# Kernel tuning notes

Measured on AMD Instinct MI355X. Metric: run time of the kernel, lower is better.

## Reference

```python
import jax, jax.numpy as jnp
import numpy as np

ALPHA = 0.2  # leaky_relu negative slope
NEG_INF = -1e18


def setup_inputs() -> dict:
    key = jax.random.key(0)
    ks = jax.random.split(key, 7)
    B, N, E = 32, 1024, 768
    OUT, MLP = 256, 2
    sent_emb = jax.random.normal(ks[0], (B, N, E), dtype=jnp.float32)
    batch_e = jnp.sort(jax.random.randint(ks[1], (B, 4), 0, N), axis=-1)
    # xavier-ish scaled weights
    W_w = jax.random.normal(ks[2], (OUT, E), dtype=jnp.float32) * (1.0 / np.sqrt(E))
    W_b = jax.random.normal(ks[3], (OUT,), dtype=jnp.float32) * 0.02
    a_w = jax.random.normal(ks[4], (1, 2 * OUT), dtype=jnp.float32) * (1.0 / np.sqrt(2 * OUT))
    mlp_w = jax.random.normal(ks[5], (MLP, OUT), dtype=jnp.float32) * (1.0 / np.sqrt(OUT))
    mlp_b = jax.random.normal(ks[6], (MLP,), dtype=jnp.float32) * 0.02
    return {"sent_emb": sent_emb, "batch_e": batch_e, "W_w": W_w, "W_b": W_b,
            "a_w": a_w, "mlp_w": mlp_w, "mlp_b": mlp_b}


def reference(sent_emb, batch_e, W_w, W_b, a_w, mlp_w, mlp_b):
    B, N, E = sent_emb.shape
    OUT = W_w.shape[0]
    # Wh = W(sent_emb): [B, N, OUT]
    Wh = jnp.einsum('bne,oe->bno', sent_emb, W_w) + W_b
    # a_T([H1 || H2]) decomposes: a1 . Wh_i + a2 . Wh_j (avoids [N,N,2*OUT] concat)
    a1, a2 = a_w[0, :OUT], a_w[0, OUT:]
    s1 = Wh @ a1  # [B, N]
    s2 = Wh @ a2  # [B, N]
    e = jax.nn.leaky_relu(s1[:, :, None] + s2[:, None, :], negative_slope=ALPHA)  # [B,N,N]
    # event mask: 0.9 inside [e1s,e1e)x[e2s,e2e), 0.1 elsewhere (both > 0, kept for fidelity)
    idx = jnp.arange(N)
    row_in = (idx[None, :] >= batch_e[:, 0:1]) & (idx[None, :] < batch_e[:, 1:2])  # [B,N]
    col_in = (idx[None, :] >= batch_e[:, 2:3]) & (idx[None, :] < batch_e[:, 3:4])  # [B,N]
    event_mask = jnp.where(row_in[:, :, None] & col_in[:, None, :], 0.9, 0.1)
    masked_e = jnp.where(event_mask > 0, e, NEG_INF)
    attn = jax.nn.softmax(masked_e, axis=-1)  # [B,N,N]
    h_prime = jax.nn.elu(jnp.einsum('bnm,bmo->bno', attn, Wh))  # [B,N,OUT]
    pooled = jnp.mean(h_prime, axis=1)  # avg_pooling over nodes -> [B,OUT]
    return pooled @ mlp_w.T + mlp_b  # [B, mlp_size]
```

## Files before the change

### kernel.cpp

```cpp
#include <hip/hip_runtime.h>
#include <hip/hip_bf16.h>

#define LOG2E 1.4426950408889634f

typedef short bfrag8 __attribute__((ext_vector_type(8)));
typedef float accf4 __attribute__((ext_vector_type(4)));

__device__ __forceinline__ unsigned pack2(float a, float b) {
    __hip_bfloat162 h = __float22bfloat162_rn(make_float2(a, b));
    return *(unsigned*)&h;
}
__device__ __forceinline__ float bflo(unsigned u) { return __uint_as_float(u << 16); }
__device__ __forceinline__ float bfhi(unsigned u) { return __uint_as_float(u & 0xFFFF0000u); }

__device__ __forceinline__ void gload_lds16(const void* g, void* lds) {
    __builtin_amdgcn_global_load_lds(
        (const __attribute__((address_space(1))) unsigned int*)g,
        (__attribute__((address_space(3))) unsigned int*)lds, 16, 0, 0);
}

__global__ __launch_bounds__(256) void convW_kernel(
    const float* __restrict__ Ww, unsigned short* __restrict__ WwB)
{
    const int id = (blockIdx.x * 256 + threadIdx.x) * 8;
    float4 a = *(const float4*)&Ww[id];
    float4 b = *(const float4*)&Ww[id + 4];
    uint4 pk;
    pk.x = pack2(a.x, a.y); pk.y = pack2(a.z, a.w);
    pk.z = pack2(b.x, b.y); pk.w = pack2(b.z, b.w);
    *(uint4*)&WwB[id] = pk;
}

__global__ __launch_bounds__(512) void gemm1_kernel(
    const float* __restrict__ sent, const unsigned short* __restrict__ WwB,
    const float* __restrict__ Wb, const float* __restrict__ aw,
    unsigned short* __restrict__ WhT, float* __restrict__ s1g,
    float* __restrict__ s2g)
{
    __shared__ char SMEM[131072];
    const int brow = blockIdx.x;
    const int t = threadIdx.x;
    const int lane = t & 63, w = t >> 6;
    const int wr = w >> 2, wc = w & 3;
    const int l15 = lane & 15, l4 = lane >> 4;
    const float* abase = sent + (size_t)brow * 128 * 768;

    accf4 acc[4][4];
#pragma unroll
    for (int i = 0; i < 4; ++i)
#pragma unroll
        for (int j = 0; j < 4; ++j)
            acc[i][j] = (accf4){0.f, 0.f, 0.f, 0.f};

    auto STAGE = [&](int buf, int k0) {
#pragma unroll
        for (int q = 0; q < 4; ++q) {
            const int id = (q << 9) + t;
            const int row = id >> 4, c = id & 15;
            gload_lds16(abase + (size_t)row * 768 + k0 + ((c ^ (row & 15)) << 2),
                        SMEM + (buf << 15) + (id << 4));
        }
#pragma unroll
        for (int q = 0; q < 4; ++q) {
            const int id = (q << 9) + t;
            const int col = id >> 3, c = id & 7;
            gload_lds16(WwB + (size_t)col * 768 + k0 + ((c ^ (col & 7)) << 3),
                        SMEM + 65536 + (buf << 15) + (id << 4));
        }
    };

    auto COMPUTE = [&](int buf) {
        const float* Ab = (const float*)(SMEM + (buf << 15));
        const unsigned short* Bb = (const unsigned short*)(SMEM + 65536 + (buf << 15));
#pragma unroll
        for (int kk = 0; kk < 2; ++kk) {
            bfrag8 af[4], bf[4];
#pragma unroll
            for (int mi = 0; mi < 4; ++mi) {
                const int row = (wr << 6) + (mi << 4) + l15;
                const int s0 = (kk << 3) + (l4 << 1);
                float4 a0 = *(const float4*)(Ab + (row << 6) + ((s0 ^ (row & 15)) << 2));
                float4 a1 = *(const float4*)(Ab + (row << 6) + (((s0 + 1) ^ (row & 15)) << 2));
                uint4 pk;
                pk.x = pack2(a0.x, a0.y); pk.y = pack2(a0.z, a0.w);
                pk.z = pack2(a1.x, a1.y); pk.w = pack2(a1.z, a1.w);
                af[mi] = *(bfrag8*)&pk;
            }
#pragma unroll
            for (int ni = 0; ni < 4; ++ni) {
                const int col = (wc << 6) + (ni << 4) + l15;
                const int s = (kk << 2) + l4;
                bf[ni] = *(const bfrag8*)(Bb + (col << 6) + ((s ^ (col & 7)) << 3));
            }
#pragma unroll
            for (int mi = 0; mi < 4; ++mi)
#pragma unroll
                for (int ni = 0; ni < 4; ++ni)
                    acc[mi][ni] = __builtin_amdgcn_mfma_f32_16x16x32_bf16(
                        af[mi], bf[ni], acc[mi][ni], 0, 0, 0);
        }
    };

    STAGE(0, 0);
    __syncthreads();
    for (int it = 0; it < 12; ++it) {
        if (it < 11) STAGE((it + 1) & 1, (it + 1) << 6);
        COMPUTE(it & 1);
        __syncthreads();
    }

    unsigned short (*T)[136] = (unsigned short(*)[136])SMEM;
    float (*sb1)[4] = (float(*)[4])(SMEM + 98304);
    float (*sb2)[4] = (float(*)[4])(SMEM + 100352);
    float sp1[16], sp2[16];
#pragma unroll
    for (int i = 0; i < 16; ++i) { sp1[i] = 0.f; sp2[i] = 0.f; }
#pragma unroll
    for (int ni = 0; ni < 4; ++ni) {
        const int colL = (wc << 6) + (ni << 4) + l15;
        const float wb  = Wb[colL];
        const float a1c = aw[colL] * LOG2E;
        const float a2c = aw[256 + colL] * LOG2E;
#pragma unroll
        for (int mi = 0; mi < 4; ++mi) {
            const int rowL = (wr << 6) + (mi << 4) + (l4 << 2);
            float v0 = acc[mi][ni][0] + wb, v1 = acc[mi][ni][1] + wb;
            float v2 = acc[mi][ni][2] + wb, v3 = acc[mi][ni][3] + wb;
            uint2 pk; pk.x = pack2(v0, v1); pk.y = pack2(v2, v3);
            *(uint2*)&T[colL][rowL] = pk;
            sp1[mi * 4 + 0] += v0 * a1c; sp1[mi * 4 + 1] += v1 * a1c;
            sp1[mi * 4 + 2] += v2 * a1c; sp1[mi * 4 + 3] += v3 * a1c;
            sp2[mi * 4 + 0] += v0 * a2c; sp2[mi * 4 + 1] += v1 * a2c;
            sp2[mi * 4 + 2] += v2 * a2c; sp2[mi * 4 + 3] += v3 * a2c;
        }
    }
#pragma unroll
    for (int d = 1; d < 16; d <<= 1)
#pragma unroll
        for (int i = 0; i < 16; ++i) {
            sp1[i] += __shfl_xor(sp1[i], d);
            sp2[i] += __shfl_xor(sp2[i], d);
        }
    if (l15 == 0)
#pragma unroll
        for (int mi = 0; mi < 4; ++mi)
#pragma unroll
            for (int reg = 0; reg < 4; ++reg) {
                const int rowL = (wr << 6) + (mi << 4) + (l4 << 2) + reg;
                sb1[rowL][wc] = sp1[mi * 4 + reg];
                sb2[rowL][wc] = sp2[mi * 4 + reg];
            }
    __syncthreads();
    {
        const int b = brow >> 3, m0 = (brow & 7) << 7;
        const int col = t >> 1, half = t & 1;
        unsigned short* dst = &WhT[(((size_t)b * 256 + col) << 10) + m0 + (half << 6)];
        const unsigned short* srcT = &T[col][half << 6];
#pragma unroll
        for (int q = 0; q < 8; ++q)
            *(uint4*)(dst + (q << 3)) = *(const uint4*)(srcT + (q << 3));
    }
    if (t < 128) {
        const int grow = brow * 128 + t;
        s1g[grow] = sb1[t][0] + sb1[t][1] + sb1[t][2] + sb1[t][3];
        s2g[grow] = sb2[t][0] + sb2[t][1] + sb2[t][2] + sb2[t][3];
    }
}

__global__ __launch_bounds__(512) void flash_kernel(
    const unsigned short* __restrict__ WhT, const float* __restrict__ s1g,
    const float* __restrict__ s2g, float* __restrict__ ppart)
{
    __shared__ char SMEM[98304];
    __shared__ float s2s[1024];
    __shared__ float zfull[128];
    __shared__ float wred[8];
    __shared__ float psum[2][256];
    const int bid0 = blockIdx.x;
    const int wg = ((bid0 & 7) << 5) + (bid0 >> 3);
    const int b = wg >> 3, nt = wg & 7, n0 = nt << 7;
    const int t = threadIdx.x;
    const int lane = t & 63, w = t >> 6;
    const int wr = w >> 2, wc = w & 3;
    const int l15 = lane & 15, l4 = lane >> 4;
    const int prow = t >> 2, pc0 = (t & 3) << 1;
    const unsigned short* wbase = WhT + ((size_t)b << 18);

    {
        const int i = t << 1;
        *(float2*)&s2s[i] = *(const float2*)&s2g[(b << 10) + i];
    }
    auto STAGEB = [&](int buf, int m0) {
#pragma unroll
        for (int q = 0; q < 4; ++q) {
            const int id = (q << 9) + t;
            const int col = id >> 3, c = id & 7;
            gload_lds16(wbase + ((size_t)col << 10) + m0 + ((c ^ (col & 7)) << 3),
                        SMEM + (buf << 15) + (id << 4));
        }
    };
    STAGEB(0, 0);
    const float s1r = s1g[(b << 10) + n0 + prow];
    __syncthreads();
    float mm = fmaxf(s2s[t], s2s[t + 512]);
#pragma unroll
    for (int d = 1; d < 64; d <<= 1) mm = fmaxf(mm, __shfl_xor(mm, d));
    if (lane == 0) wred[w] = mm;
    __syncthreads();
    float s2mx = wred[0];
#pragma unroll
    for (int i = 1; i < 8; ++i) s2mx = fmaxf(s2mx, wred[i]);
    const float xm = s1r + s2mx;
    const float Mr = fmaxf(xm, 0.2f * xm);

    accf4 acc[4][4];
#pragma unroll
    for (int i = 0; i < 4; ++i)
#pragma unroll
        for (int j = 0; j < 4; ++j)
            acc[i][j] = (accf4){0.f, 0.f, 0.f, 0.f};
    float zp = 0.f;

    auto PCOMP = [&](int buf, int mt) {
        const float* sp = &s2s[(mt << 6) + (pc0 << 3)];
        float4 x0 = *(const float4*)sp;
        float4 x1 = *(const float4*)(sp + 4);
        float4 x2 = *(const float4*)(sp + 8);
        float4 x3 = *(const float4*)(sp + 12);
        float xs[16] = {x0.x, x0.y, x0.z, x0.w, x1.x, x1.y, x1.z, x1.w,
                        x2.x, x2.y, x2.z, x2.w, x3.x, x3.y, x3.z, x3.w};
        unsigned u[8];
#pragma unroll
        for (int j = 0; j < 8; ++j) {
            float a = s1r + xs[2 * j], c = s1r + xs[2 * j + 1];
            a = fmaxf(a, 0.2f * a) - Mr;
            c = fmaxf(c, 0.2f * c) - Mr;
            u[j] = pack2(__builtin_amdgcn_exp2f(a), __builtin_amdgcn_exp2f(c));
            zp += bflo(u[j]) + bfhi(u[j]);
        }
        char* pb = SMEM + 65536 + (buf << 14) + (prow << 7);
        uint4 k0; k0.x = u[0]; k0.y = u[1]; k0.z = u[2]; k0.w = u[3];
        uint4 k1; k1.x = u[4]; k1.y = u[5]; k1.z = u[6]; k1.w = u[7];
        *(uint4*)(pb + ((pc0 ^ (prow & 7)) << 4)) = k0;
        *(uint4*)(pb + (((pc0 + 1) ^ (prow & 7)) << 4)) = k1;
    };
    auto MM = [&](int buf) {
        const unsigned short* Bb = (const unsigned short*)(SMEM + (buf << 15));
        const char* Pb = SMEM + 65536 + (buf << 14);
#pragma unroll
        for (int kk = 0; kk < 2; ++kk) {
            bfrag8 af[4], bf[4];
#pragma unroll
            for (int mi = 0; mi < 4; ++mi) {
                const int row = (wr << 6) + (mi << 4) + l15;
                const int s = (kk << 2) + l4;
                af[mi] = *(const bfrag8*)(Pb + (row << 7) + ((s ^ (row & 7)) << 4));
            }
#pragma unroll
            for (int ni = 0; ni < 4; ++ni) {
                const int col = (wc << 6) + (ni << 4) + l15;
                const int s = (kk << 2) + l4;
                bf[ni] = *(const bfrag8*)(Bb + (col << 6) + ((s ^ (col & 7)) << 3));
            }
#pragma unroll
            for (int mi = 0; mi < 4; ++mi)
#pragma unroll
                for (int ni = 0; ni < 4; ++ni)
                    acc[mi][ni] = __builtin_amdgcn_mfma_f32_16x16x32_bf16(
                        af[mi], bf[ni], acc[mi][ni], 0, 0, 0);
        }
    };

    PCOMP(0, 0);
    __syncthreads();
    for (int mt = 0; mt < 16; ++mt) {
        if (mt < 15) {
            STAGEB((mt + 1) & 1, (mt + 1) << 6);
            PCOMP((mt + 1) & 1, mt + 1);
        }
        MM(mt & 1);
        __syncthreads();
    }

    zp += __shfl_xor(zp, 1);
    zp += __shfl_xor(zp, 2);
    if ((lane & 3) == 0) zfull[prow] = zp;
    __syncthreads();

    float rz[16];
#pragma unroll
    for (int mi = 0; mi < 4; ++mi)
#pragma unroll
        for (int r = 0; r < 4; ++r)
            rz[mi * 4 + r] = 1.0f / zfull[(wr << 6) + (mi << 4) + (l4 << 2) + r];
#pragma unroll
    for (int ni = 0; ni < 4; ++ni) {
        float cs = 0.f;
#pragma unroll
        for (int mi = 0; mi < 4; ++mi)
#pragma unroll
            for (int r = 0; r < 4; ++r) {
                float v = acc[mi][ni][r] * rz[mi * 4 + r];
                cs += v > 0.f ? v : (__expf(v) - 1.0f);
            }
        cs += __shfl_xor(cs, 16);
        cs += __shfl_xor(cs, 32);
        if (l4 == 0) psum[wr][(wc << 6) + (ni << 4) + l15] = cs;
    }
    __syncthreads();
    if (t < 256)
        ppart[(((size_t)b << 3) + nt) * 256 + t] = psum[0][t] + psum[1][t];
}

__global__ __launch_bounds__(256) void final_kernel(
    const float* __restrict__ ppart, const float* __restrict__ mlpw,
    const float* __restrict__ mlpb, float* __restrict__ out)
{
    __shared__ float r0[4], r1[4];
    const int b = blockIdx.x, t = threadIdx.x;
    float p = 0.f;
#pragma unroll
    for (int nt = 0; nt < 8; ++nt)
        p += ppart[(((size_t)b << 3) + nt) * 256 + t];
    float m0 = p * mlpw[t], m1 = p * mlpw[256 + t];
#pragma unroll
    for (int d = 1; d < 64; d <<= 1) {
        m0 += __shfl_xor(m0, d);
        m1 += __shfl_xor(m1, d);
    }
    if ((t & 63) == 0) { r0[t >> 6] = m0; r1[t >> 6] = m1; }
    __syncthreads();
    if (t == 0) out[b * 2 + 0] = (r0[0] + r0[1] + r0[2] + r0[3]) * (1.f / 1024.f) + mlpb[0];
    if (t == 1) out[b * 2 + 1] = (r1[0] + r1[1] + r1[2] + r1[3]) * (1.f / 1024.f) + mlpb[1];
}

extern "C" void kernel_launch(void* const* d_in, const int* in_sizes, int n_in,
                              void* d_out, int out_size, void* d_ws, size_t ws_size,
                              hipStream_t stream) {
    const float* sent = (const float*)d_in[0];
    const float* Ww   = (const float*)d_in[2];
    const float* Wb   = (const float*)d_in[3];
    const float* aw   = (const float*)d_in[4];
    const float* mlpw = (const float*)d_in[5];
    const float* mlpb = (const float*)d_in[6];
    float* out = (float*)d_out;

    char* ws = (char*)d_ws;
    unsigned short* WhT  = (unsigned short*)ws;
    unsigned short* WwB  = (unsigned short*)(ws + 16777216);
    float*          s1g  = (float*)(ws + 17170432);
    float*          s2g  = s1g + 32768;
    float*          ppart= s2g + 32768;

    convW_kernel<<<96, 256, 0, stream>>>(Ww, WwB);
    gemm1_kernel<<<256, 512, 0, stream>>>(sent, WwB, Wb, aw, WhT, s1g, s2g);
    flash_kernel<<<256, 512, 0, stream>>>(WhT, s1g, s2g, ppart);
    final_kernel<<<32, 256, 0, stream>>>(ppart, mlpw, mlpb, out);
}
```

Baseline: 204.2 us.

## Drop weight conversion kernel; convert to bf16 in registers before LDS staging

Removes the separate convW kernel and reads fp32 W directly in gemm1. A and W tiles are now loaded into registers, packed to bf16, and written to LDS, replacing the direct global-to-LDS async loads of fp32 A. This halves LDS footprint and removes per-MFMA fp32->bf16 conversion from LDS reads, at the cost of register-staged loads that are less asynchronous. Each block re-reads and re-converts fp32 W, so W traffic doubles per block.

Result: slower. 219.0 us (+7.3%).

```diff
diff --git a/kernel.cpp b/kernel.cpp
--- a/kernel.cpp
+++ b/kernel.cpp
@@ -19,25 +19,13 @@
         (__attribute__((address_space(3))) unsigned int*)lds, 16, 0, 0);
 }
 
-__global__ __launch_bounds__(256) void convW_kernel(
-    const float* __restrict__ Ww, unsigned short* __restrict__ WwB)
-{
-    const int id = (blockIdx.x * 256 + threadIdx.x) * 8;
-    float4 a = *(const float4*)&Ww[id];
-    float4 b = *(const float4*)&Ww[id + 4];
-    uint4 pk;
-    pk.x = pack2(a.x, a.y); pk.y = pack2(a.z, a.w);
-    pk.z = pack2(b.x, b.y); pk.w = pack2(b.z, b.w);
-    *(uint4*)&WwB[id] = pk;
-}
-
 __global__ __launch_bounds__(512) void gemm1_kernel(
-    const float* __restrict__ sent, const unsigned short* __restrict__ WwB,
+    const float* __restrict__ sent, const float* __restrict__ Ww,
     const float* __restrict__ Wb, const float* __restrict__ aw,
     unsigned short* __restrict__ WhT, float* __restrict__ s1g,
     float* __restrict__ s2g)
 {
-    __shared__ char SMEM[131072];
+    __shared__ char SMEM[98304];
     const int brow = blockIdx.x;
     const int t = threadIdx.x;
     const int lane = t & 63, w = t >> 6;
@@ -45,6 +33,9 @@
     const int l15 = lane & 15, l4 = lane >> 4;
     const float* abase = sent + (size_t)brow * 128 * 768;
 
+    const int ar = t >> 2, ac2 = (t & 3) << 1;
+    const int bc = t >> 1, bh = t & 1;
+
     accf4 acc[4][4];
 #pragma unroll
     for (int i = 0; i < 4; ++i)
@@ -52,45 +43,55 @@
         for (int j = 0; j < 4; ++j)
             acc[i][j] = (accf4){0.f, 0.f, 0.f, 0.f};
 
-    auto STAGE = [&](int buf, int k0) {
+    float4 aL[4], bL[8];
+    auto LOADR = [&](int k0) {
+        const float* ap = abase + ar * 768 + k0 + (ac2 << 3);
+#pragma unroll
+        for (int q = 0; q < 4; ++q) aL[q] = *(const float4*)(ap + (q << 2));
+        const float* bp = Ww + bc * 768 + k0 + (bh << 5);
+#pragma unroll
+        for (int q = 0; q < 8; ++q) bL[q] = *(const float4*)(bp + (q << 2));
+    };
+    auto WRITE = [&](int buf) {
+        char* Asb = SMEM + (buf << 14);
+#pragma unroll
+        for (int q = 0; q < 2; ++q) {
+            uint4 pk;
+            pk.x = pack2(aL[2 * q].x, aL[2 * q].y);
+            pk.y = pack2(aL[2 * q].z, aL[2 * q].w);
+            pk.z = pack2(aL[2 * q + 1].x, aL[2 * q + 1].y);
+            pk.w = pack2(aL[2 * q + 1].z, aL[2 * q + 1].w);
+            const int c = ac2 + q;
+            *(uint4*)(Asb + (ar << 7) + ((c ^ (ar & 7)) << 4)) = pk;
+        }
+        char* Bsb = SMEM + 32768 + (buf << 15);
 #pragma unroll
         for (int q = 0; q < 4; ++q) {
-            const int id = (q << 9) + t;
-            const int row = id >> 4, c = id & 15;
-            gload_lds16(abase + (size_t)row * 768 + k0 + ((c ^ (row & 15)) << 2),
-                        SMEM + (buf << 15) + (id << 4));
-        }
-#pragma unroll
-        for (int q = 0; q < 4; ++q) {
-            const int id = (q << 9) + t;
-            const int col = id >> 3, c = id & 7;
-            gload_lds16(WwB + (size_t)col * 768 + k0 + ((c ^ (col & 7)) << 3),
-                        SMEM + 65536 + (buf << 15) + (id << 4));
-        }
-    };
-
+            uint4 pk;
+            pk.x = pack2(bL[2 * q].x, bL[2 * q].y);
+            pk.y = pack2(bL[2 * q].z, bL[2 * q].w);
+            pk.z = pack2(bL[2 * q + 1].x, bL[2 * q + 1].y);
+            pk.w = pack2(bL[2 * q + 1].z, bL[2 * q + 1].w);
+            const int c = (bh << 2) + q;
+            *(uint4*)(Bsb + (bc << 7) + ((c ^ (bc & 7)) << 4)) = pk;
+        }
+    };
     auto COMPUTE = [&](int buf) {
-        const float* Ab = (const float*)(SMEM + (buf << 15));
-        const unsigned short* Bb = (const unsigned short*)(SMEM + 65536 + (buf << 15));
+        const char* Ab = SMEM + (buf << 14);
+        const char* Bb = SMEM + 32768 + (buf << 15);
 #pragma unroll
         for (int kk = 0; kk < 2; ++kk) {
+            const int s = (kk << 2) + l4;
             bfrag8 af[4], bf[4];
 #pragma unroll
             for (int mi = 0; mi < 4; ++mi) {
                 const int row = (wr << 6) + (mi << 4) + l15;
-                const int s0 = (kk << 3) + (l4 << 1);
-                float4 a0 = *(const float4*)(Ab + (row << 6) + ((s0 ^ (row & 15)) << 2));
-                float4 a1 = *(const float4*)(Ab + (row << 6) + (((s0 + 1) ^ (row & 15)) << 2));
-                uint4 pk;
-                pk.x = pack2(a0.x, a0.y); pk.y = pack2(a0.z, a0.w);
-                pk.z = pack2(a1.x, a1.y); pk.w = pack2(a1.z, a1.w);
-                af[mi] = *(bfrag8*)&pk;
+                af[mi] = *(const bfrag8*)(Ab + (row << 7) + ((s ^ (row & 7)) << 4));
             }
 #pragma unroll
             for (int ni = 0; ni < 4; ++ni) {
                 const int col = (wc << 6) + (ni << 4) + l15;
-                const int s = (kk << 2) + l4;
-                bf[ni] = *(const bfrag8*)(Bb + (col << 6) + ((s ^ (col & 7)) << 3));
+                bf[ni] = *(const bfrag8*)(Bb + (col << 7) + ((s ^ (col & 7)) << 4));
             }
 #pragma unroll
             for (int mi = 0; mi < 4; ++mi)
@@ -101,17 +102,19 @@
         }
     };
 
-    STAGE(0, 0);
+    LOADR(0);
+    WRITE(0);
     __syncthreads();
     for (int it = 0; it < 12; ++it) {
-        if (it < 11) STAGE((it + 1) & 1, (it + 1) << 6);
+        if (it < 11) LOADR((it + 1) << 6);
         COMPUTE(it & 1);
+        if (it < 11) WRITE((it + 1) & 1);
         __syncthreads();
     }
 
     unsigned short (*T)[136] = (unsigned short(*)[136])SMEM;
-    float (*sb1)[4] = (float(*)[4])(SMEM + 98304);
-    float (*sb2)[4] = (float(*)[4])(SMEM + 100352);
+    float (*sb1)[4] = (float(*)[4])(SMEM + 90112);
+    float (*sb2)[4] = (float(*)[4])(SMEM + 92160);
     float sp1[16], sp2[16];
 #pragma unroll
     for (int i = 0; i < 16; ++i) { sp1[i] = 0.f; sp2[i] = 0.f; }
@@ -245,22 +248,21 @@
         *(uint4*)(pb + (((pc0 + 1) ^ (prow & 7)) << 4)) = k1;
     };
     auto MM = [&](int buf) {
-        const unsigned short* Bb = (const unsigned short*)(SMEM + (buf << 15));
+        const char* Bb = SMEM + (buf << 15);
         const char* Pb = SMEM + 65536 + (buf << 14);
 #pragma unroll
         for (int kk = 0; kk < 2; ++kk) {
+            const int s = (kk << 2) + l4;
             bfrag8 af[4], bf[4];
 #pragma unroll
             for (int mi = 0; mi < 4; ++mi) {
                 const int row = (wr << 6) + (mi << 4) + l15;
-                const int s = (kk << 2) + l4;
                 af[mi] = *(const bfrag8*)(Pb + (row << 7) + ((s ^ (row & 7)) << 4));
             }
 #pragma unroll
             for (int ni = 0; ni < 4; ++ni) {
                 const int col = (wc << 6) + (ni << 4) + l15;
-                const int s = (kk << 2) + l4;
-                bf[ni] = *(const bfrag8*)(Bb + (col << 6) + ((s ^ (col & 7)) << 3));
+                bf[ni] = *(const bfrag8*)(Bb + (col << 7) + ((s ^ (col & 7)) << 4));
             }
 #pragma unroll
             for (int mi = 0; mi < 4; ++mi)
@@ -347,13 +349,11 @@
 
     char* ws = (char*)d_ws;
     unsigned short* WhT  = (unsigned short*)ws;
-    unsigned short* WwB  = (unsigned short*)(ws + 16777216);
-    float*          s1g  = (float*)(ws + 17170432);
+    float*          s1g  = (float*)(ws + 16777216);
     float*          s2g  = s1g + 32768;
     float*          ppart= s2g + 32768;
 
-    convW_kernel<<<96, 256, 0, stream>>>(Ww, WwB);
-    gemm1_kernel<<<256, 512, 0, stream>>>(sent, WwB, Wb, aw, WhT, s1g, s2g);
+    gemm1_kernel<<<256, 512, 0, stream>>>(sent, Ww, Wb, aw, WhT, s1g, s2g);
     flash_kernel<<<256, 512, 0, stream>>>(WhT, s1g, s2g, ppart);
     final_kernel<<<32, 256, 0, stream>>>(ppart, mlpw, mlpb, out);
 }
```
